# Performance work log

Measured on AMD Instinct MI355X. Metric: run time of the kernel, lower is better.

Reference implementation:

```python
import jax, jax.numpy as jnp
import numpy as np

N = 100_000      # nodes
E = 1_600_000    # edges (avg degree 16)
D_IN = 64        # node feature dim
H = 128          # hidden
E_IN = 64        # edge feature dim
C = 8            # num classes
EPS = 1e-5       # BatchNorm eps


def setup_inputs() -> dict:
    key = jax.random.key(0)
    ks = jax.random.split(key, 22)
    w = lambda k, shape: jax.random.normal(k, shape, dtype=jnp.float32) * 0.05
    return {
        "x_nodes": jax.random.normal(ks[0], (N, D_IN), dtype=jnp.float32),
        "e_feat": jax.random.normal(ks[1], (E, E_IN), dtype=jnp.float32),
        # SAGE layer 1 (fc_self, fc_neigh, bias)
        "Ws1": w(ks[2], (D_IN, H)), "Wn1": w(ks[3], (D_IN, H)), "b1": w(ks[4], (H,)),
        "g1": 1.0 + 0.1 * jax.random.normal(ks[5], (H,), dtype=jnp.float32),
        "bt1": 0.1 * jax.random.normal(ks[6], (H,), dtype=jnp.float32),
        # SAGE layer 2
        "Ws2": w(ks[7], (H, H)), "Wn2": w(ks[8], (H, H)), "b2": w(ks[9], (H,)),
        "g2": 1.0 + 0.1 * jax.random.normal(ks[10], (H,), dtype=jnp.float32),
        "bt2": 0.1 * jax.random.normal(ks[11], (H,), dtype=jnp.float32),
        # Edge MLP
        "We1": w(ks[12], (2 * H + E_IN, H)), "be1": w(ks[13], (H,)),
        "We2": w(ks[14], (H, C)), "be2": w(ks[15], (C,)),
        # Graph structure (message-flow graph, reused for both layers) and pair graph
        "src": jax.random.randint(ks[16], (E,), 0, N, dtype=jnp.int32),
        "dst": jax.random.randint(ks[17], (E,), 0, N, dtype=jnp.int32),
        "u": jax.random.randint(ks[18], (E,), 0, N, dtype=jnp.int32),
        "v": jax.random.randint(ks[19], (E,), 0, N, dtype=jnp.int32),
    }


def _sage_mean(h, src, dst, inv_deg, Ws, Wn, b):
    # DGL SAGEConv('mean'): rst = fc_self(h_dst) + fc_neigh(mean_{in-neighbors} h_src) + bias
    agg = jax.ops.segment_sum(h[src], dst, num_segments=h.shape[0]) * inv_deg[:, None]
    return h @ Ws + agg @ Wn + b


def _bn_relu(h, gamma, beta):
    # BatchNorm1d (training-mode batch stats, biased variance) + ReLU
    mu = h.mean(axis=0)
    var = jnp.mean((h - mu) ** 2, axis=0)
    return jax.nn.relu((h - mu) * jax.lax.rsqrt(var + EPS) * gamma + beta)


def reference(x_nodes, e_feat, Ws1, Wn1, b1, g1, bt1, Ws2, Wn2, b2, g2, bt2,
              We1, be1, We2, be2, src, dst, u, v):
    n = x_nodes.shape[0]
    deg = jax.ops.segment_sum(jnp.ones_like(src, dtype=x_nodes.dtype), dst, num_segments=n)
    inv_deg = jnp.where(deg > 0, 1.0 / jnp.maximum(deg, 1.0), 0.0)  # zero-degree -> 0 (DGL mean)
    h = _bn_relu(_sage_mean(x_nodes, src, dst, inv_deg, Ws1, Wn1, b1), g1, bt1)
    h = _bn_relu(_sage_mean(h, src, dst, inv_deg, Ws2, Wn2, b2), g2, bt2)
    # edge head: gather endpoints, concat with edge features, MLP (dropout = eval identity)
    e_repr = jnp.concatenate([h[u], h[v], e_feat], axis=1)  # [E, 2H + E_IN]
    hid = jax.nn.relu(e_repr @ We1 + be1)
    return hid @ We2 + be2
```

## Files before the change

kernel.cpp:

```cpp
#include <hip/hip_runtime.h>

#define NN 100000
#define EE 1600000
constexpr float BN_EPS = 1e-5f;

typedef __attribute__((ext_vector_type(8))) short short8;
typedef __attribute__((ext_vector_type(4))) float f32x4;

__device__ __forceinline__ short f2bf(float f) {
    unsigned u = __float_as_uint(f);
    u += 0x7fff + ((u >> 16) & 1);
    return (short)(u >> 16);
}
__device__ __forceinline__ float bf2f(short s) {
    return __uint_as_float(((unsigned)(unsigned short)s) << 16);
}

typedef __attribute__((address_space(1))) const unsigned int guint;
typedef __attribute__((address_space(3))) unsigned int luint;
__device__ __forceinline__ void gload_lds16(const void* g, void* l) {
    __builtin_amdgcn_global_load_lds((guint*)g, (luint*)l, 16, 0, 0);
}

__global__ void k_count(const int* __restrict__ dst, int* __restrict__ cnt) {
    int e = blockIdx.x * 256 + threadIdx.x;
    if (e < EE) atomicAdd(&cnt[dst[e]], 1);
}

__global__ __launch_bounds__(1024) void k_scan_part(const int* __restrict__ cnt,
                                                    int* __restrict__ bsum) {
    const int t = threadIdx.x, lane = t & 63, w = t >> 6;
    int i = blockIdx.x * 1024 + t;
    int v = (i < NN) ? cnt[i] : 0;
#pragma unroll
    for (int d = 1; d < 64; d <<= 1) v += __shfl_xor(v, d, 64);
    __shared__ int ws[16];
    if (lane == 0) ws[w] = v;
    __syncthreads();
    if (t == 0) {
        int s = 0;
#pragma unroll
        for (int k = 0; k < 16; ++k) s += ws[k];
        bsum[blockIdx.x] = s;
    }
}

__global__ void k_scan_base(int* __restrict__ bsum, int* __restrict__ offs, int nb) {
    if (threadIdx.x == 0) {
        int run = 0;
        for (int k = 0; k < nb; ++k) {
            int v = bsum[k];
            bsum[k] = run;
            run += v;
        }
        offs[NN] = run;
    }
}

__global__ __launch_bounds__(1024) void k_scan_final(const int* __restrict__ cnt,
                                                     const int* __restrict__ bsum,
                                                     int* __restrict__ offs,
                                                     int* __restrict__ cursor,
                                                     float* __restrict__ invd) {
    const int t = threadIdx.x, lane = t & 63, w = t >> 6;
    __shared__ int wsum[16], wexcl[16];
    int i = blockIdx.x * 1024 + t;
    int v = (i < NN) ? cnt[i] : 0;
    int s = v;
#pragma unroll
    for (int d = 1; d < 64; d <<= 1) {
        int o = __shfl_up(s, d, 64);
        if (lane >= d) s += o;
    }
    if (lane == 63) wsum[w] = s;
    __syncthreads();
    if (t < 16) {
        int wv = wsum[t];
        int ss = wv;
#pragma unroll
        for (int d = 1; d < 16; d <<= 1) {
            int o = __shfl_up(ss, d, 16);
            if (t >= d) ss += o;
        }
        wexcl[t] = ss - wv;
    }
    __syncthreads();
    if (i < NN) {
        int o = bsum[blockIdx.x] + (s - v) + wexcl[w];
        offs[i] = o;
        cursor[i] = o;
        invd[i] = v > 0 ? 1.f / (float)v : 0.f;
    }
}

__global__ void k_fill(const int* __restrict__ src, const int* __restrict__ dst,
                       int* __restrict__ cursor, int* __restrict__ eidsrc) {
    int e = blockIdx.x * 256 + threadIdx.x;
    if (e < EE) {
        int pos = atomicAdd(&cursor[dst[e]], 1);
        eidsrc[pos] = src[e];
    }
}

__global__ void k_f2bf(const float* __restrict__ in, short* __restrict__ out, int n8) {
    int i = blockIdx.x * 256 + threadIdx.x;
    if (i >= n8) return;
    float4 a = ((const float4*)in)[i * 2];
    float4 b = ((const float4*)in)[i * 2 + 1];
    short8 o;
    o[0] = f2bf(a.x); o[1] = f2bf(a.y); o[2] = f2bf(a.z); o[3] = f2bf(a.w);
    o[4] = f2bf(b.x); o[5] = f2bf(b.y); o[6] = f2bf(b.z); o[7] = f2bf(b.w);
    ((short8*)out)[i] = o;
}

template <int F>
__global__ __launch_bounds__(256) void k_gather_bf(
    const short* __restrict__ hbsrc, const int* __restrict__ offs,
    const int* __restrict__ eidsrc, const float* __restrict__ invd,
    short* __restrict__ aggb) {
    constexpr int G = F / 8;
    int gid = blockIdx.x * 256 + threadIdx.x;
    int node = gid / G;
    int sub = gid % G;
    if (node >= NN) return;
    int beg = offs[node], end = offs[node + 1];
    float iv = invd[node];
    float s[8] = {0.f, 0.f, 0.f, 0.f, 0.f, 0.f, 0.f, 0.f};
    const size_t co = (size_t)sub * 8;
    int p = beg;
    for (; p + 4 <= end; p += 4) {
        int i0 = eidsrc[p], i1 = eidsrc[p + 1], i2 = eidsrc[p + 2], i3 = eidsrc[p + 3];
        short8 r0 = *(const short8*)(hbsrc + (size_t)i0 * F + co);
        short8 r1 = *(const short8*)(hbsrc + (size_t)i1 * F + co);
        short8 r2 = *(const short8*)(hbsrc + (size_t)i2 * F + co);
        short8 r3 = *(const short8*)(hbsrc + (size_t)i3 * F + co);
#pragma unroll
        for (int j = 0; j < 8; ++j)
            s[j] += (bf2f(r0[j]) + bf2f(r1[j])) + (bf2f(r2[j]) + bf2f(r3[j]));
    }
    for (; p < end; ++p) {
        short8 r = *(const short8*)(hbsrc + (size_t)eidsrc[p] * F + co);
#pragma unroll
        for (int j = 0; j < 8; ++j) s[j] += bf2f(r[j]);
    }
    short8 o;
#pragma unroll
    for (int j = 0; j < 8; ++j) o[j] = f2bf(s[j] * iv);
    *(short8*)(aggb + (size_t)node * F + co) = o;
}

__device__ __forceinline__ void packW(const float* W, short* Wp, int local, int kbase) {
    int k = local >> 7, col = local & 127;
    int gk = k + kbase;
    int kc = gk >> 5, kw = gk & 31, bp = kw >> 3, j = kw & 7;
    int cb = col >> 4, n = col & 15;
    Wp[kc * 4096 + (cb * 64 + bp * 16 + n) * 8 + j] = f2bf(W[k * 128 + col]);
}

__global__ void k_pack_all(const float* __restrict__ We1, const float* __restrict__ Ws1,
                           const float* __restrict__ Wn1, const float* __restrict__ Ws2,
                           const float* __restrict__ Wn2, const float* __restrict__ We2,
                           short* __restrict__ Wp_e, short* __restrict__ Wp1,
                           short* __restrict__ Wp2, short* __restrict__ Wp2e) {
    int idx = blockIdx.x * 256 + threadIdx.x;
    if (idx < 40960) {
        packW(We1, Wp_e, idx, 0);
    } else if (idx < 49152) {
        packW(Ws1, Wp1, idx - 40960, 0);
    } else if (idx < 57344) {
        packW(Wn1, Wp1, idx - 49152, 64);
    } else if (idx < 73728) {
        packW(Ws2, Wp2, idx - 57344, 0);
    } else if (idx < 90112) {
        packW(Wn2, Wp2, idx - 73728, 128);
    } else if (idx < 92160) {
        int local = idx - 90112;
        int k = local >> 4, n = local & 15;
        float val = (n < 8) ? We2[k * 8 + n] : 0.f;
        int kc2 = k >> 5, kl = k & 31, bp = kl >> 3, j = kl & 7;
        Wp2e[(kc2 * 64 + bp * 16 + n) * 8 + j] = f2bf(val);
    }
}

template <int KC1, int KC2>
__global__ __launch_bounds__(256) void k_node_mfma(
    const short* __restrict__ A1, const short* __restrict__ A2,
    const short* __restrict__ Wp, const float* __restrict__ bias,
    float* __restrict__ outf, float* __restrict__ stats) {
    __shared__ __align__(16) short sbuf[16384];
    __shared__ float bs[128];
    __shared__ float reds[4][128], redss[4][128];
    const int t = threadIdx.x;
    if (t < 128) bs[t] = bias[t];
    const int rowbase = blockIdx.x * 128;
    const int lane = t & 63, w = t >> 6;
    const int fo = (lane >> 4) * 16 + (lane & 15);

    auto NSTAGE = [&](int kc, short* Ad, short* Bd) {
        const short* src;
        int kst, kloc;
        if (kc < KC1) { src = A1; kst = KC1 * 32; kloc = kc * 32; }
        else          { src = A2; kst = KC2 * 32; kloc = (kc - KC1) * 32; }
#pragma unroll
        for (int p = 0; p < 2; ++p) {
            int s = t + p * 256;
            int b = (s >> 4) & 3;
            int row = rowbase + ((s >> 6) << 4) + (s & 15);
            gload_lds16(src + (size_t)row * kst + kloc + b * 8, Ad + s * 8);
            gload_lds16(Wp + (size_t)kc * 4096 + s * 8, Bd + s * 8);
        }
    };

    f32x4 acc[2][8];
#pragma unroll
    for (int i = 0; i < 2; ++i)
#pragma unroll
        for (int j = 0; j < 8; ++j) acc[i][j] = (f32x4){0.f, 0.f, 0.f, 0.f};

    constexpr int KC = KC1 + KC2;
    NSTAGE(0, sbuf, sbuf + 4096);
    __syncthreads();
    for (int kc = 0; kc < KC; ++kc) {
        const int cur = kc & 1;
        short* Ac = sbuf + (cur ? 8192 : 0);
        short* Bc = Ac + 4096;
        if (kc + 1 < KC) {
            short* An = sbuf + (cur ? 0 : 8192);
            NSTAGE(kc + 1, An, An + 4096);
        }
        short8 a0 = *(const short8*)(Ac + (2 * w * 64 + fo) * 8);
        short8 a1 = *(const short8*)(Ac + ((2 * w + 1) * 64 + fo) * 8);
#pragma unroll
        for (int cb = 0; cb < 8; ++cb) {
            short8 bfr = *(const short8*)(Bc + (cb * 64 + fo) * 8);
            acc[0][cb] = __builtin_amdgcn_mfma_f32_16x16x32_bf16(a0, bfr, acc[0][cb], 0, 0, 0);
            acc[1][cb] = __builtin_amdgcn_mfma_f32_16x16x32_bf16(a1, bfr, acc[1][cb], 0, 0, 0);
        }
        __syncthreads();
    }

    float cs[8], css[8];
#pragma unroll
    for (int cb = 0; cb < 8; ++cb) { cs[cb] = 0.f; css[cb] = 0.f; }
#pragma unroll
    for (int rb2 = 0; rb2 < 2; ++rb2) {
        int rloc = 32 * w + rb2 * 16 + ((lane >> 4) << 2);
#pragma unroll
        for (int cb = 0; cb < 8; ++cb) {
            int col = cb * 16 + (lane & 15);
            float bb = bs[col];
#pragma unroll
            for (int i = 0; i < 4; ++i) {
                int row = rowbase + rloc + i;
                if (row < NN) {
                    float v = acc[rb2][cb][i] + bb;
                    outf[(size_t)row * 128 + col] = v;
                    cs[cb] += v;
                    css[cb] += v * v;
                }
            }
        }
    }
#pragma unroll
    for (int cb = 0; cb < 8; ++cb) {
        cs[cb] += __shfl_xor(cs[cb], 16);
        cs[cb] += __shfl_xor(cs[cb], 32);
        css[cb] += __shfl_xor(css[cb], 16);
        css[cb] += __shfl_xor(css[cb], 32);
    }
    if (lane < 16) {
#pragma unroll
        for (int cb = 0; cb < 8; ++cb) {
            reds[w][cb * 16 + lane] = cs[cb];
            redss[w][cb * 16 + lane] = css[cb];
        }
    }
    __syncthreads();
    if (t < 128) {
        atomicAdd(&stats[t], reds[0][t] + reds[1][t] + reds[2][t] + reds[3][t]);
    } else {
        int c = t - 128;
        atomicAdd(&stats[128 + c], redss[0][c] + redss[1][c] + redss[2][c] + redss[3][c]);
    }
}

__global__ void k_bnrelu_bf16(const float* __restrict__ h, const float* __restrict__ stats,
                              const float* __restrict__ g, const float* __restrict__ bt,
                              short* __restrict__ hb) {
    __shared__ float a_sh[128], b_sh[128];
    const int t = threadIdx.x;
    if (t < 128) {
        float mu = stats[t] * (1.f / NN);
        float var = stats[128 + t] * (1.f / NN) - mu * mu;
        float a = g[t] * rsqrtf(var + BN_EPS);
        a_sh[t] = a;
        b_sh[t] = bt[t] - mu * a;
    }
    __syncthreads();
    int gid = blockIdx.x * 256 + t;
    if (gid >= NN * 16) return;
    int c0 = (gid & 15) * 8;
    float4 v0 = reinterpret_cast<const float4*>(h)[gid * 2];
    float4 v1 = reinterpret_cast<const float4*>(h)[gid * 2 + 1];
    short8 o;
    o[0] = f2bf(fmaxf(fmaf(a_sh[c0 + 0], v0.x, b_sh[c0 + 0]), 0.f));
    o[1] = f2bf(fmaxf(fmaf(a_sh[c0 + 1], v0.y, b_sh[c0 + 1]), 0.f));
    o[2] = f2bf(fmaxf(fmaf(a_sh[c0 + 2], v0.z, b_sh[c0 + 2]), 0.f));
    o[3] = f2bf(fmaxf(fmaf(a_sh[c0 + 3], v0.w, b_sh[c0 + 3]), 0.f));
    o[4] = f2bf(fmaxf(fmaf(a_sh[c0 + 4], v1.x, b_sh[c0 + 4]), 0.f));
    o[5] = f2bf(fmaxf(fmaf(a_sh[c0 + 5], v1.y, b_sh[c0 + 5]), 0.f));
    o[6] = f2bf(fmaxf(fmaf(a_sh[c0 + 6], v1.z, b_sh[c0 + 6]), 0.f));
    o[7] = f2bf(fmaxf(fmaf(a_sh[c0 + 7], v1.w, b_sh[c0 + 7]), 0.f));
    reinterpret_cast<short8*>(hb)[gid] = o;
}

__global__ __launch_bounds__(256) void k_edge_mfma(
    const short* __restrict__ hb, const float* __restrict__ ef,
    const short* __restrict__ Wp, const short* __restrict__ Wp2e,
    const float* __restrict__ be1, const float* __restrict__ be2,
    const int* __restrict__ uu, const int* __restrict__ vv,
    float* __restrict__ out) {
    __shared__ __align__(16) short smem[17408];
    __shared__ float be1s[128];
    __shared__ int suv[256];
    short* A_l = smem;
    short* B_l = smem + 4096;
    const int t = threadIdx.x;
    const int eb = blockIdx.x * 128;
    if (t < 128) {
        suv[t] = uu[eb + t];
        suv[128 + t] = vv[eb + t];
        be1s[t] = be1[t];
    }
    __syncthreads();

    const int lane = t & 63, w = t >> 6;
    const int fo = (lane >> 4) * 16 + (lane & 15);
    const int srow = t >> 1;
    const int sb0 = (t & 1) * 2;
    const int sslotbase = (srow >> 4) * 64 + (srow & 15);

    short8 b2f[4];
#pragma unroll
    for (int kc2 = 0; kc2 < 4; ++kc2)
        b2f[kc2] = *(const short8*)(Wp2e + (kc2 * 64 + fo) * 8);

    f32x4 acc[2][8];
#pragma unroll
    for (int i = 0; i < 2; ++i)
#pragma unroll
        for (int j = 0; j < 8; ++j) acc[i][j] = (f32x4){0.f, 0.f, 0.f, 0.f};

    for (int kc = 0; kc < 10; ++kc) {
        if (kc < 8) {
#pragma unroll
            for (int p = 0; p < 2; ++p) {
                int s = t + p * 256;
                int b = (s >> 4) & 3;
                int row = ((s >> 6) << 4) + (s & 15);
                const short* gsrc =
                    hb + (size_t)suv[(kc >= 4) * 128 + row] * 128 + (kc & 3) * 32 + b * 8;
                gload_lds16(gsrc, A_l + s * 8);
            }
        } else {
            const float* er = ef + (size_t)(eb + srow) * 64 + (kc - 8) * 32;
#pragma unroll
            for (int p = 0; p < 2; ++p) {
                int b = sb0 + p;
                float4 f0 = *(const float4*)(er + b * 8);
                float4 f1 = *(const float4*)(er + b * 8 + 4);
                short8 v8;
                v8[0] = f2bf(f0.x); v8[1] = f2bf(f0.y);
                v8[2] = f2bf(f0.z); v8[3] = f2bf(f0.w);
                v8[4] = f2bf(f1.x); v8[5] = f2bf(f1.y);
                v8[6] = f2bf(f1.z); v8[7] = f2bf(f1.w);
                *(short8*)(A_l + (sslotbase + b * 16) * 8) = v8;
            }
        }
#pragma unroll
        for (int p = 0; p < 2; ++p) {
            int s = t + p * 256;
            gload_lds16(Wp + (size_t)kc * 4096 + s * 8, B_l + s * 8);
        }
        __syncthreads();

        short8 afr0 = *(const short8*)(A_l + ((2 * w) * 64 + fo) * 8);
        short8 afr1 = *(const short8*)(A_l + ((2 * w + 1) * 64 + fo) * 8);
#pragma unroll
        for (int cb = 0; cb < 8; ++cb) {
            short8 bfr = *(const short8*)(B_l + (cb * 64 + fo) * 8);
            acc[0][cb] = __builtin_amdgcn_mfma_f32_16x16x32_bf16(afr0, bfr, acc[0][cb], 0, 0, 0);
            acc[1][cb] = __builtin_amdgcn_mfma_f32_16x16x32_bf16(afr1, bfr, acc[1][cb], 0, 0, 0);
        }
        __syncthreads();
    }

    short* Hid = smem;
#pragma unroll
    for (int rb2 = 0; rb2 < 2; ++rb2)
#pragma unroll
        for (int cb = 0; cb < 8; ++cb) {
            int col = cb * 16 + (lane & 15);
            int rbase = 32 * w + rb2 * 16 + ((lane >> 4) << 2);
            float bb = be1s[col];
#pragma unroll
            for (int i = 0; i < 4; ++i)
                Hid[(rbase + i) * 136 + col] = f2bf(fmaxf(acc[rb2][cb][i] + bb, 0.f));
        }
    __syncthreads();

#pragma unroll
    for (int rf = 0; rf < 2; ++rf) {
        f32x4 a2 = (f32x4){0.f, 0.f, 0.f, 0.f};
        const int rbl = 32 * w + 16 * rf + (lane & 15);
#pragma unroll
        for (int kc2 = 0; kc2 < 4; ++kc2) {
            short8 af = *(const short8*)(Hid + rbl * 136 + kc2 * 32 + 8 * (lane >> 4));
            a2 = __builtin_amdgcn_mfma_f32_16x16x32_bf16(af, b2f[kc2], a2, 0, 0, 0);
        }
        int col = lane & 15;
        if (col < 8) {
            int r0 = eb + 32 * w + 16 * rf + 4 * (lane >> 4);
            float bb = be2[col];
#pragma unroll
            for (int i = 0; i < 4; ++i)
                out[(size_t)(r0 + i) * 8 + col] = a2[i] + bb;
        }
    }
}

extern "C" void kernel_launch(void* const* d_in, const int* in_sizes, int n_in,
                              void* d_out, int out_size, void* d_ws, size_t ws_size,
                              hipStream_t stream) {
    const float* x   = (const float*)d_in[0];
    const float* ef  = (const float*)d_in[1];
    const float* Ws1 = (const float*)d_in[2];
    const float* Wn1 = (const float*)d_in[3];
    const float* b1  = (const float*)d_in[4];
    const float* g1  = (const float*)d_in[5];
    const float* bt1 = (const float*)d_in[6];
    const float* Ws2 = (const float*)d_in[7];
    const float* Wn2 = (const float*)d_in[8];
    const float* b2  = (const float*)d_in[9];
    const float* g2  = (const float*)d_in[10];
    const float* bt2 = (const float*)d_in[11];
    const float* We1 = (const float*)d_in[12];
    const float* be1 = (const float*)d_in[13];
    const float* We2 = (const float*)d_in[14];
    const float* be2 = (const float*)d_in[15];
    const int* src = (const int*)d_in[16];
    const int* dst = (const int*)d_in[17];
    const int* u   = (const int*)d_in[18];
    const int* v   = (const int*)d_in[19];
    float* out = (float*)d_out;

    char* p = (char*)d_ws;
    auto take = [&](size_t bytes) {
        char* r = p;
        p += (bytes + 255) & ~(size_t)255;
        return r;
    };
    int* cnt     = (int*)take(NN * 4);
    float* stats = (float*)take(512 * 4);
    float* invd  = (float*)take(NN * 4);
    int* offs    = (int*)take((NN + 1) * 4);
    int* cursor  = (int*)take(NN * 4);
    int* bsum    = (int*)take(128 * 4);
    int* eidsrc  = (int*)take((size_t)EE * 4);
    short* Wp_e  = (short*)take(320 * 128 * 2);
    short* Wp1   = (short*)take(128 * 128 * 2);
    short* Wp2   = (short*)take(256 * 128 * 2);
    short* Wp2e  = (short*)take(256 * 8 * 2);
    short* xb    = (short*)take((size_t)NN * 64 * 2);
    short* agg1b = (short*)take((size_t)NN * 64 * 2);
    short* h1b   = (short*)take((size_t)NN * 128 * 2);
    short* agg2b = (short*)take((size_t)NN * 128 * 2);
    take(65536);
    float* h1 = out;
    float* h2 = out;
    short* hb = xb;

    const int NB = (NN + 1023) / 1024;

    hipMemsetAsync(cnt, 0, ((char*)stats - (char*)cnt) + 512 * 4, stream);
    k_count<<<(EE + 255) / 256, 256, 0, stream>>>(dst, cnt);
    k_scan_part<<<NB, 1024, 0, stream>>>(cnt, bsum);
    k_scan_base<<<1, 64, 0, stream>>>(bsum, offs, NB);
    k_scan_final<<<NB, 1024, 0, stream>>>(cnt, bsum, offs, cursor, invd);
    k_fill<<<(EE + 255) / 256, 256, 0, stream>>>(src, dst, cursor, eidsrc);
    k_pack_all<<<360, 256, 0, stream>>>(We1, Ws1, Wn1, Ws2, Wn2, We2, Wp_e, Wp1, Wp2, Wp2e);
    k_f2bf<<<(NN * 8 + 255) / 256, 256, 0, stream>>>(x, xb, NN * 8);

    k_gather_bf<64><<<(NN * 8 + 255) / 256, 256, 0, stream>>>(xb, offs, eidsrc, invd, agg1b);
    k_node_mfma<2, 2><<<(NN + 127) / 128, 256, 0, stream>>>(xb, agg1b, Wp1, b1, h1, stats);
    k_bnrelu_bf16<<<(NN * 16 + 255) / 256, 256, 0, stream>>>(h1, stats, g1, bt1, h1b);

    k_gather_bf<128><<<(NN * 16 + 255) / 256, 256, 0, stream>>>(h1b, offs, eidsrc, invd, agg2b);
    k_node_mfma<4, 4><<<(NN + 127) / 128, 256, 0, stream>>>(h1b, agg2b, Wp2, b2, h2, stats + 256);
    k_bnrelu_bf16<<<(NN * 16 + 255) / 256, 256, 0, stream>>>(h2, stats + 256, g2, bt2, hb);

    k_edge_mfma<<<EE / 128, 256, 0, stream>>>(hb, ef, Wp_e, Wp2e, be1, be2, u, v, out);
}
```

Measured before the change: 662.0 us.

## Double-buffer edge MLP LDS staging and unroll neighbor gather by eight

The edge MLP kernel now splits shared memory into two A/B buffers. It issues the loads for the next K-chunk before running the MFMAs on the current one, and drops one of the two barriers per iteration, so global latency is meant to overlap with matrix math. Separately, the mean-aggregation gather gains an 8-wide unrolled loop so more independent row loads are in flight per thread. The costs are more register pressure in both kernels and reliance on the async LDS loads being complete at the single barrier.

```diff
diff --git a/kernel.cpp b/kernel.cpp
--- a/kernel.cpp
+++ b/kernel.cpp
@@ -128,6 +128,19 @@
     float s[8] = {0.f, 0.f, 0.f, 0.f, 0.f, 0.f, 0.f, 0.f};
     const size_t co = (size_t)sub * 8;
     int p = beg;
+    for (; p + 8 <= end; p += 8) {
+        int idx[8];
+#pragma unroll
+        for (int q = 0; q < 8; ++q) idx[q] = eidsrc[p + q];
+        short8 r[8];
+#pragma unroll
+        for (int q = 0; q < 8; ++q)
+            r[q] = *(const short8*)(hbsrc + (size_t)idx[q] * F + co);
+#pragma unroll
+        for (int q = 0; q < 8; ++q)
+#pragma unroll
+            for (int j = 0; j < 8; ++j) s[j] += bf2f(r[q][j]);
+    }
     for (; p + 4 <= end; p += 4) {
         int i0 = eidsrc[p], i1 = eidsrc[p + 1], i2 = eidsrc[p + 2], i3 = eidsrc[p + 3];
         short8 r0 = *(const short8*)(hbsrc + (size_t)i0 * F + co);
@@ -323,8 +336,6 @@
     __shared__ __align__(16) short smem[17408];
     __shared__ float be1s[128];
     __shared__ int suv[256];
-    short* A_l = smem;
-    short* B_l = smem + 4096;
     const int t = threadIdx.x;
     const int eb = blockIdx.x * 128;
     if (t < 128) {
@@ -345,13 +356,7 @@
     for (int kc2 = 0; kc2 < 4; ++kc2)
         b2f[kc2] = *(const short8*)(Wp2e + (kc2 * 64 + fo) * 8);
 
-    f32x4 acc[2][8];
-#pragma unroll
-    for (int i = 0; i < 2; ++i)
-#pragma unroll
-        for (int j = 0; j < 8; ++j) acc[i][j] = (f32x4){0.f, 0.f, 0.f, 0.f};
-
-    for (int kc = 0; kc < 10; ++kc) {
+    auto STAGE = [&](int kc, short* Ad, short* Bd) {
         if (kc < 8) {
 #pragma unroll
             for (int p = 0; p < 2; ++p) {
@@ -360,7 +365,7 @@
                 int row = ((s >> 6) << 4) + (s & 15);
                 const short* gsrc =
                     hb + (size_t)suv[(kc >= 4) * 128 + row] * 128 + (kc & 3) * 32 + b * 8;
-                gload_lds16(gsrc, A_l + s * 8);
+                gload_lds16(gsrc, Ad + s * 8);
             }
         } else {
             const float* er = ef + (size_t)(eb + srow) * 64 + (kc - 8) * 32;
@@ -374,21 +379,36 @@
                 v8[2] = f2bf(f0.z); v8[3] = f2bf(f0.w);
                 v8[4] = f2bf(f1.x); v8[5] = f2bf(f1.y);
                 v8[6] = f2bf(f1.z); v8[7] = f2bf(f1.w);
-                *(short8*)(A_l + (sslotbase + b * 16) * 8) = v8;
+                *(short8*)(Ad + (sslotbase + b * 16) * 8) = v8;
             }
         }
 #pragma unroll
         for (int p = 0; p < 2; ++p) {
             int s = t + p * 256;
-            gload_lds16(Wp + (size_t)kc * 4096 + s * 8, B_l + s * 8);
-        }
-        __syncthreads();
-
-        short8 afr0 = *(const short8*)(A_l + ((2 * w) * 64 + fo) * 8);
-        short8 afr1 = *(const short8*)(A_l + ((2 * w + 1) * 64 + fo) * 8);
+            gload_lds16(Wp + (size_t)kc * 4096 + s * 8, Bd + s * 8);
+        }
+    };
+
+    f32x4 acc[2][8];
+#pragma unroll
+    for (int i = 0; i < 2; ++i)
+#pragma unroll
+        for (int j = 0; j < 8; ++j) acc[i][j] = (f32x4){0.f, 0.f, 0.f, 0.f};
+
+    STAGE(0, smem, smem + 4096);
+    __syncthreads();
+    for (int kc = 0; kc < 10; ++kc) {
+        short* Ac = smem + (kc & 1) * 8192;
+        short* Bc = Ac + 4096;
+        if (kc < 9) {
+            short* An = smem + ((kc + 1) & 1) * 8192;
+            STAGE(kc + 1, An, An + 4096);
+        }
+        short8 afr0 = *(const short8*)(Ac + ((2 * w) * 64 + fo) * 8);
+        short8 afr1 = *(const short8*)(Ac + ((2 * w + 1) * 64 + fo) * 8);
 #pragma unroll
         for (int cb = 0; cb < 8; ++cb) {
-            short8 bfr = *(const short8*)(B_l + (cb * 64 + fo) * 8);
+            short8 bfr = *(const short8*)(Bc + (cb * 64 + fo) * 8);
             acc[0][cb] = __builtin_amdgcn_mfma_f32_16x16x32_bf16(afr0, bfr, acc[0][cb], 0, 0, 0);
             acc[1][cb] = __builtin_amdgcn_mfma_f32_16x16x32_bf16(afr1, bfr, acc[1][cb], 0, 0, 0);
         }
```

Measured after the change: 656.3 us. About the same (-0.9%).
